# Kernel tuning notes

Measured on AMD Instinct MI355X. Metric: run time of the kernel, lower is better.

Reference implementation:

```python
import jax, jax.numpy as jnp
import numpy as np

HEADS, DIM_HEAD, NEIGHBORS = 8, 64, 64
REL_DIST_SCALE, REL_DIST_CUTOFF, THETA, EPS = 100.0, 5000.0, 10000.0, 1e-8


def _rotate_half(x):
    # interleaved pairs: (x0,x1),(x2,x3),... -> (-x1,x0),(-x3,x2),...
    xp = x.reshape(*x.shape[:-1], -1, 2)
    a, b = xp[..., 0], xp[..., 1]
    return jnp.stack((-b, a), axis=-1).reshape(x.shape)


def _apply_rotary(t, freqs):
    return t * jnp.cos(freqs) + _rotate_half(t) * jnp.sin(freqs)


def _gelu(x):
    return jax.nn.gelu(x, approximate=False)  # torch nn.GELU default = exact erf


def setup_inputs() -> dict:
    key = jax.random.key(0)
    ks = jax.random.split(key, 12)
    b, n, d, e = 2, 2048, 256, 16
    h, dh = HEADS, DIM_HEAD
    inner = h * dh
    std = 0.02
    return {
        "feats": jax.random.normal(ks[0], (b, n, d), jnp.float32),
        "coors": jax.random.normal(ks[1], (b, n, 3), jnp.float32),
        "edges": jax.random.normal(ks[2], (b, n, n, e), jnp.float32),
        "W_qkv": jax.random.normal(ks[3], (d, inner * 3), jnp.float32) * std,
        "W_out": jax.random.normal(ks[4], (inner, d), jnp.float32) * std,
        "b_out": jnp.zeros((d,), jnp.float32),
        "W_e1": jax.random.normal(ks[5], (h + e, 2 * (h + e)), jnp.float32) * std,
        "b_e1": jnp.zeros((2 * (h + e),), jnp.float32),
        "W_e2": jax.random.normal(ks[6], (2 * (h + e), h), jnp.float32) * std,
        "b_e2": jnp.zeros((h,), jnp.float32),
        "W_c": jax.random.normal(ks[7], (h, h), jnp.float32) * std,
        "b_c": jnp.zeros((h,), jnp.float32),
        "W_g": jax.random.normal(ks[8], (h, h), jnp.float32) * std,
        "b_g": jnp.zeros((h,), jnp.float32),
        "coors_combine": jax.random.normal(ks[9], (h,), jnp.float32),
        "coors_scale": jnp.ones((1,), jnp.float32),
    }


def reference(feats, coors, edges, W_qkv, W_out, b_out, W_e1, b_e1, W_e2, b_e2,
              W_c, b_c, W_g, b_g, coors_combine, coors_scale):
    b, n, d = feats.shape
    h, dh, nn_k = HEADS, DIM_HEAD, NEIGHBORS

    # pairwise relative coordinates / distances (O(n^2) irregular part)
    rel_coors = coors[:, :, None, :] - coors[:, None, :, :]            # b n n 3
    rel_dist = jnp.linalg.norm(rel_coors, axis=-1)                      # b n n

    # topk nearest neighbors (largest=False -> top_k of negated distances)
    _, nbhd_idx = jax.lax.top_k(-rel_dist, nn_k)                        # b n nn

    qkv = feats @ W_qkv                                                 # b n 3*h*dh
    q, k, v = jnp.split(qkv, 3, axis=-1)
    q = q.reshape(b, n, h, dh).transpose(0, 2, 1, 3)                    # b h n dh
    k = k.reshape(b, n, h, dh).transpose(0, 2, 1, 3)
    v = v.reshape(b, n, h, dh).transpose(0, 2, 1, 3)

    # batched_index_select gathers
    k = jax.vmap(lambda kb, ib: kb[:, ib])(k, nbhd_idx)                 # b h n nn dh
    v = jax.vmap(lambda vb, ib: vb[:, ib])(v, nbhd_idx)                 # b h n nn dh
    rel_dist_nb = jnp.take_along_axis(rel_dist, nbhd_idx, axis=2)       # b n nn
    rel_coors_nb = jnp.take_along_axis(rel_coors, nbhd_idx[..., None], axis=2)  # b n nn 3
    edges_nb = jnp.take_along_axis(edges, nbhd_idx[..., None], axis=2)  # b n nn e

    # rotary on relative distances; q's freqs are zeros -> identity rotation (skipped)
    inv_freq = 1.0 / (THETA ** (jnp.arange(0, dh, 2, dtype=jnp.float32) / dh))
    t = jnp.minimum(rel_dist_nb * REL_DIST_SCALE, REL_DIST_CUTOFF)
    freqs = jnp.repeat(t[..., None] * inv_freq, 2, axis=-1)[:, None]    # b 1 n nn dh
    k = _apply_rotary(k, freqs)
    v = _apply_rotary(v, freqs)

    # edges provided -> no 1/sqrt(dh) scale, then edge MLP
    qk = jnp.einsum('bhid,bhijd->bhij', q, k)                           # b h i j
    qk = jnp.transpose(qk, (0, 2, 3, 1))                                # b i j h
    x = jnp.concatenate([qk, edges_nb], axis=-1)                        # b i j (h+e)
    qk = _gelu(x @ W_e1 + b_e1) @ W_e2 + b_e2                           # b i j h

    # coordinate attention branch (coors_mlp = GELU + Linear when edges exist)
    coor_weights = _gelu(qk) @ W_c + b_c                                # b i j h
    coor_attn = jax.nn.softmax(coor_weights, axis=2)                    # softmax over j
    gate = jnp.tanh(qk @ W_g + b_g)                                     # b i j h

    nrm = jnp.linalg.norm(rel_coors_nb, axis=-1, keepdims=True)
    rel_normed = rel_coors_nb / jnp.maximum(nrm, EPS) * coors_scale     # b i j 3

    rel_out = jnp.einsum('bijh,bijc->bich', coor_attn * gate, rel_normed)
    coors_delta = jnp.einsum('bich,h->bic', rel_out, coors_combine)     # b n 3

    # feature attention branch
    attn = jax.nn.softmax(jnp.transpose(qk, (0, 3, 1, 2)), axis=-1)     # b h i j
    out = jnp.einsum('bhij,bhijd->bhid', attn, v)
    out = out.transpose(0, 2, 1, 3).reshape(b, n, h * dh)
    node_out = out @ W_out + b_out                                      # b n d
    return node_out, coors_delta
```

## Files before the change

kernel.cpp:

```cpp
#include <hip/hip_runtime.h>
#include <hip/hip_fp16.h>
#include <math.h>

#define NPTS 2048
#define NB 64
#define H 8
#define DH 64
#define INNER 512

__device__ __forceinline__ float gelu_exact(float x) {
  return 0.5f * x * (1.0f + erff(x * 0.7071067811865475f));
}

__device__ __forceinline__ unsigned int pack_cs(float c, float s) {
  __half2 h = __floats2half2_rn(c, s);
  return *reinterpret_cast<unsigned int*>(&h);
}
__device__ __forceinline__ float2 unpack_cs(unsigned int u) {
  __half2 h = *reinterpret_cast<__half2*>(&u);
  return __half22float2(h);
}

__global__ __launch_bounds__(256) void topk_kernel(const float* __restrict__ coors,
                                                   int* __restrict__ nbhd) {
  const int row = blockIdx.x;
  const int b = row >> 11;
  const int tid = threadIdx.x;
  __shared__ unsigned long long red[4];
  __shared__ unsigned long long winner;
  const float* cb = coors + (size_t)b * NPTS * 3;
  const float cx = coors[(size_t)row * 3 + 0];
  const float cy = coors[(size_t)row * 3 + 1];
  const float cz = coors[(size_t)row * 3 + 2];
  unsigned long long keys[8];
#pragma unroll
  for (int s = 0; s < 8; ++s) {
    const int j = tid + (s << 8);
    const float dx = cx - cb[j * 3 + 0];
    const float dy = cy - cb[j * 3 + 1];
    const float dz = cz - cb[j * 3 + 2];
    const float d = sqrtf(dx * dx + dy * dy + dz * dz);
    keys[s] = (((unsigned long long)__float_as_uint(d)) << 32) | (unsigned long long)j;
  }
  for (int it = 0; it < NB; ++it) {
    unsigned long long k = ~0ull;
#pragma unroll
    for (int s = 0; s < 8; ++s) k = keys[s] < k ? keys[s] : k;
#pragma unroll
    for (int off = 32; off > 0; off >>= 1) {
      unsigned long long o = __shfl_xor(k, off, 64);
      k = o < k ? o : k;
    }
    if ((tid & 63) == 0) red[tid >> 6] = k;
    __syncthreads();
    if (tid == 0) {
      unsigned long long w = red[0];
      for (int q = 1; q < 4; ++q) w = red[q] < w ? red[q] : w;
      winner = w;
      nbhd[(size_t)row * NB + it] = (int)(w & 0xffffffffull);
    }
    __syncthreads();
    const unsigned long long w = winner;
#pragma unroll
    for (int s = 0; s < 8; ++s)
      if (keys[s] == w) keys[s] = ~0ull;
  }
}

__global__ __launch_bounds__(256) void gemm_tiled(const float* __restrict__ A,
                                                  const float* __restrict__ B,
                                                  const float* __restrict__ bias,
                                                  float* __restrict__ C,
                                                  int M, int N, int K) {
  __shared__ float As[16][68];
  __shared__ float Bs[16][68];
  const int tid = threadIdx.x;
  const int tx = tid & 15;
  const int ty = tid >> 4;
  const int n0 = blockIdx.x << 6;
  const int m0 = blockIdx.y << 6;
  const int la_m = tid >> 2;
  const int la_k = (tid & 3) << 2;
  const int lb_k = tid >> 4;
  const int lb_n = (tid & 15) << 2;
  float acc[4][4] = {{0.f}};
  for (int kk = 0; kk < K; kk += 16) {
    const float4 a4 = *(const float4*)(A + (size_t)(m0 + la_m) * K + kk + la_k);
    const float4 b4 = *(const float4*)(B + (size_t)(kk + lb_k) * N + n0 + lb_n);
    As[la_k + 0][la_m] = a4.x;
    As[la_k + 1][la_m] = a4.y;
    As[la_k + 2][la_m] = a4.z;
    As[la_k + 3][la_m] = a4.w;
    *(float4*)(&Bs[lb_k][lb_n]) = b4;
    __syncthreads();
#pragma unroll
    for (int k = 0; k < 16; ++k) {
      const float4 av = *(const float4*)(&As[k][ty << 2]);
      const float4 bv = *(const float4*)(&Bs[k][tx << 2]);
      acc[0][0] += av.x * bv.x; acc[0][1] += av.x * bv.y; acc[0][2] += av.x * bv.z; acc[0][3] += av.x * bv.w;
      acc[1][0] += av.y * bv.x; acc[1][1] += av.y * bv.y; acc[1][2] += av.y * bv.z; acc[1][3] += av.y * bv.w;
      acc[2][0] += av.z * bv.x; acc[2][1] += av.z * bv.y; acc[2][2] += av.z * bv.z; acc[2][3] += av.z * bv.w;
      acc[3][0] += av.w * bv.x; acc[3][1] += av.w * bv.y; acc[3][2] += av.w * bv.z; acc[3][3] += av.w * bv.w;
    }
    __syncthreads();
  }
#pragma unroll
  for (int r = 0; r < 4; ++r) {
#pragma unroll
    for (int c = 0; c < 4; ++c) {
      const int n = n0 + (tx << 2) + c;
      float v = acc[r][c];
      if (bias) v += bias[n];
      C[(size_t)(m0 + (ty << 2) + r) * N + n] = v;
    }
  }
}

__global__ __launch_bounds__(256, 4) void attn_kernel(
    const float* __restrict__ qkv, const float* __restrict__ coors,
    const float* __restrict__ edges, const int* __restrict__ nbhd,
    const float* __restrict__ W_e1, const float* __restrict__ b_e1,
    const float* __restrict__ W_e2, const float* __restrict__ b_e2,
    const float* __restrict__ W_c, const float* __restrict__ b_c,
    const float* __restrict__ W_g, const float* __restrict__ b_g,
    const float* __restrict__ coors_combine, const float* __restrict__ coors_scale,
    float* __restrict__ attn_out, float* __restrict__ coors_out) {
  __shared__ float q_s[H][68];
  __shared__ unsigned int cs_s[NB][33];
  __shared__ float qk_s[NB][9];
  __shared__ float qk2_s[NB][9];
  __shared__ float attn_s[NB][9];
  __shared__ float edg_s[NB][17];
  __shared__ float rel_s[NB][4];
  __shared__ float dist_s[NB];
  __shared__ int idx_s[NB];
  __shared__ float We1[24 * 48];
  __shared__ float We2[48 * 9];
  __shared__ float be1[48];
  __shared__ float be2[H], bcs[H], bgs[H], ccs[H];
  __shared__ float Wcs[H * H], Wgs[H * H];
  __shared__ float invf[32];
  __shared__ float credx[4][3];

  const int row = blockIdx.x;
  const int b = row >> 11;
  const int tid = threadIdx.x;
  const size_t qbase = (size_t)row * 1536;

  {
    int t0 = tid;
    q_s[t0 >> 6][t0 & 63] = qkv[qbase + t0];
    int t1 = tid + 256;
    q_s[t1 >> 6][t1 & 63] = qkv[qbase + t1];
  }
  for (int t = tid; t < 24 * 48; t += 256) We1[t] = W_e1[t];
  for (int t = tid; t < 48 * H; t += 256) We2[(t >> 3) * 9 + (t & 7)] = W_e2[t];
  if (tid < 48) be1[tid] = b_e1[tid];
  if (tid < H) { be2[tid] = b_e2[tid]; bcs[tid] = b_c[tid]; bgs[tid] = b_g[tid]; ccs[tid] = coors_combine[tid]; }
  if (tid < H * H) { Wcs[tid] = W_c[tid]; Wgs[tid] = W_g[tid]; }
  if (tid < 32) invf[tid] = expf(-(float)tid * 0.28782313662425575f);
  if (tid < NB) {
    const int jj = nbhd[(size_t)row * NB + tid];
    idx_s[tid] = jj;
    const float csc = coors_scale[0];
    const float dx = coors[(size_t)row * 3 + 0] - coors[((size_t)b * NPTS + jj) * 3 + 0];
    const float dy = coors[(size_t)row * 3 + 1] - coors[((size_t)b * NPTS + jj) * 3 + 1];
    const float dz = coors[(size_t)row * 3 + 2] - coors[((size_t)b * NPTS + jj) * 3 + 2];
    const float d = sqrtf(dx * dx + dy * dy + dz * dz);
    dist_s[tid] = d;
    const float inv = csc / fmaxf(d, 1e-8f);
    rel_s[tid][0] = dx * inv;
    rel_s[tid][1] = dy * inv;
    rel_s[tid][2] = dz * inv;
  }
  __syncthreads();

#pragma unroll
  for (int s = 0; s < 8; ++s) {
    const int p = tid + (s << 8);
    const int j = p >> 5, m = p & 31;
    const float t = fminf(dist_s[j] * 100.0f, 5000.0f);
    float sv, cv;
    __sincosf(t * invf[m], &sv, &cv);
    cs_s[j][m] = pack_cs(cv, sv);
  }
  {
    const size_t ebase = (size_t)row * NPTS * 16;
#pragma unroll
    for (int s = 0; s < 4; ++s) {
      const int p = tid + (s << 8);
      const int j = p >> 4, e = p & 15;
      edg_s[j][e] = edges[ebase + (size_t)idx_s[j] * 16 + e];
    }
  }
  __syncthreads();

#pragma unroll
  for (int s = 0; s < 2; ++s) {
    const int p = tid + (s << 8);
    const int j = p >> 3, h = p & 7;
    const float* krow = qkv + ((size_t)b * NPTS + idx_s[j]) * 1536 + INNER + h * DH;
    float acc = 0.f;
#pragma unroll
    for (int m4 = 0; m4 < 16; ++m4) {
      const float4 kv = *(const float4*)(krow + (m4 << 2));
      const float4 qv = *(const float4*)(&q_s[h][m4 << 2]);
      const int m = m4 << 1;
      const float2 c0 = unpack_cs(cs_s[j][m]);
      const float2 c1 = unpack_cs(cs_s[j][m + 1]);
      acc += qv.x * (kv.x * c0.x - kv.y * c0.y) + qv.y * (kv.y * c0.x + kv.x * c0.y) +
             qv.z * (kv.z * c1.x - kv.w * c1.y) + qv.w * (kv.w * c1.x + kv.z * c1.y);
    }
    qk_s[j][h] = acc;
  }
  __syncthreads();

  {
    const int j = tid >> 2, part = tid & 3;
    float hv[12];
#pragma unroll
    for (int l = 0; l < 12; ++l) {
      const int hh = part * 12 + l;
      float a = be1[hh];
#pragma unroll
      for (int r = 0; r < 8; ++r) a += qk_s[j][r] * We1[r * 48 + hh];
#pragma unroll
      for (int r = 0; r < 16; ++r) a += edg_s[j][r] * We1[(8 + r) * 48 + hh];
      hv[l] = gelu_exact(a);
    }
    float p8[8];
#pragma unroll
    for (int h = 0; h < 8; ++h) {
      float a = 0.f;
#pragma unroll
      for (int l = 0; l < 12; ++l) a += hv[l] * We2[(part * 12 + l) * 9 + h];
      a += __shfl_xor(a, 1, 64);
      a += __shfl_xor(a, 2, 64);
      p8[h] = a + be2[h];
    }
    qk2_s[j][(part << 1) + 0] = p8[(part << 1) + 0];
    qk2_s[j][(part << 1) + 1] = p8[(part << 1) + 1];
  }
  __syncthreads();

  {
    const int lane = tid & 63;
    const int wv = tid >> 6;
    float qv[8], ge[8];
#pragma unroll
    for (int r = 0; r < 8; ++r) { qv[r] = qk2_s[lane][r]; ge[r] = gelu_exact(qv[r]); }
    float wpart = 0.f;
#pragma unroll
    for (int hh = 0; hh < 2; ++hh) {
      const int h = (wv << 1) + hh;
      float y = qv[h];
      float my = y;
#pragma unroll
      for (int off = 32; off > 0; off >>= 1) my = fmaxf(my, __shfl_xor(my, off, 64));
      const float e2 = __expf(y - my);
      float s2 = e2;
#pragma unroll
      for (int off = 32; off > 0; off >>= 1) s2 += __shfl_xor(s2, off, 64);
      attn_s[lane][h] = e2 / s2;
      float cwv = bcs[h], gt = bgs[h];
#pragma unroll
      for (int r = 0; r < 8; ++r) {
        cwv += ge[r] * Wcs[r * 8 + h];
        gt += qv[r] * Wgs[r * 8 + h];
      }
      gt = tanhf(gt);
      float mx = cwv;
#pragma unroll
      for (int off = 32; off > 0; off >>= 1) mx = fmaxf(mx, __shfl_xor(mx, off, 64));
      const float e = __expf(cwv - mx);
      float sm = e;
#pragma unroll
      for (int off = 32; off > 0; off >>= 1) sm += __shfl_xor(sm, off, 64);
      wpart += (e / sm) * gt * ccs[h];
    }
    float px = wpart * rel_s[lane][0];
    float py = wpart * rel_s[lane][1];
    float pz = wpart * rel_s[lane][2];
#pragma unroll
    for (int off = 32; off > 0; off >>= 1) {
      px += __shfl_xor(px, off, 64);
      py += __shfl_xor(py, off, 64);
      pz += __shfl_xor(pz, off, 64);
    }
    if (lane == 0) { credx[wv][0] = px; credx[wv][1] = py; credx[wv][2] = pz; }
  }
  __syncthreads();

  if (tid == 0) {
    coors_out[(size_t)row * 3 + 0] = credx[0][0] + credx[1][0] + credx[2][0] + credx[3][0];
    coors_out[(size_t)row * 3 + 1] = credx[0][1] + credx[1][1] + credx[2][1] + credx[3][1];
    coors_out[(size_t)row * 3 + 2] = credx[0][2] + credx[1][2] + credx[2][2] + credx[3][2];
  }

  {
    const int h = tid >> 5, m = tid & 31;
    const size_t off_v = (size_t)(2 * INNER + h * DH + (m << 1));
    float o0 = 0.f, o1 = 0.f;
#pragma unroll 8
    for (int j = 0; j < NB; ++j) {
      const float2 v = *(const float2*)(qkv + ((size_t)b * NPTS + idx_s[j]) * 1536 + off_v);
      const float2 cs = unpack_cs(cs_s[j][m]);
      const float a = attn_s[j][h];
      o0 += a * (v.x * cs.x - v.y * cs.y);
      o1 += a * (v.y * cs.x + v.x * cs.y);
    }
    *(float2*)(attn_out + (size_t)row * INNER + h * DH + (m << 1)) = make_float2(o0, o1);
  }
}

extern "C" void kernel_launch(void* const* d_in, const int* in_sizes, int n_in,
                              void* d_out, int out_size, void* d_ws, size_t ws_size,
                              hipStream_t stream) {
  const float* feats = (const float*)d_in[0];
  const float* coors = (const float*)d_in[1];
  const float* edges = (const float*)d_in[2];
  const float* W_qkv = (const float*)d_in[3];
  const float* W_out = (const float*)d_in[4];
  const float* b_out = (const float*)d_in[5];
  const float* W_e1 = (const float*)d_in[6];
  const float* b_e1 = (const float*)d_in[7];
  const float* W_e2 = (const float*)d_in[8];
  const float* b_e2 = (const float*)d_in[9];
  const float* W_c = (const float*)d_in[10];
  const float* b_c = (const float*)d_in[11];
  const float* W_g = (const float*)d_in[12];
  const float* b_g = (const float*)d_in[13];
  const float* cc = (const float*)d_in[14];
  const float* cscale = (const float*)d_in[15];

  float* out = (float*)d_out;
  float* qkv = (float*)d_ws;
  float* attn_out = qkv + (size_t)4096 * 1536;
  int* nbhd = (int*)(attn_out + (size_t)4096 * 512);

  gemm_tiled<<<dim3(24, 64), 256, 0, stream>>>(feats, W_qkv, nullptr, qkv, 4096, 1536, 256);
  topk_kernel<<<4096, 256, 0, stream>>>(coors, nbhd);
  attn_kernel<<<4096, 256, 0, stream>>>(qkv, coors, edges, nbhd,
                                        W_e1, b_e1, W_e2, b_e2, W_c, b_c, W_g, b_g,
                                        cc, cscale, attn_out, out + (size_t)4096 * 256);
  gemm_tiled<<<dim3(4, 64), 256, 0, stream>>>(attn_out, W_out, b_out, out, 4096, 256, 512);
}
```

Measured before the change: 1.004 ms.

## Restructure top-k as per-wave sorted selection plus merge-by-rank

Each thread sorts its 8 distance keys with a sorting network. Each wave then independently extracts its 64 smallest keys by repeated shuffle-min and pop, with no block-wide barriers per iteration. A single sync follows, and the four per-wave sorted lists are merged by computing each candidate's global rank with binary searches into the other lists. This removes 128 __syncthreads and the serial single-thread reduction from the top-k loop, in exchange for more register shuffling and a merge step.

```diff
diff --git a/kernel.cpp b/kernel.cpp
--- a/kernel.cpp
+++ b/kernel.cpp
@@ -26,44 +26,68 @@
   const int row = blockIdx.x;
   const int b = row >> 11;
   const int tid = threadIdx.x;
-  __shared__ unsigned long long red[4];
-  __shared__ unsigned long long winner;
+  const int lane = tid & 63;
+  const int wv = tid >> 6;
+  __shared__ unsigned long long list[4][64];
+
   const float* cb = coors + (size_t)b * NPTS * 3;
   const float cx = coors[(size_t)row * 3 + 0];
   const float cy = coors[(size_t)row * 3 + 1];
   const float cz = coors[(size_t)row * 3 + 2];
+
   unsigned long long keys[8];
 #pragma unroll
   for (int s = 0; s < 8; ++s) {
-    const int j = tid + (s << 8);
+    const int j = (wv << 9) + (s << 6) + lane;
     const float dx = cx - cb[j * 3 + 0];
     const float dy = cy - cb[j * 3 + 1];
     const float dz = cz - cb[j * 3 + 2];
     const float d = sqrtf(dx * dx + dy * dy + dz * dz);
     keys[s] = (((unsigned long long)__float_as_uint(d)) << 32) | (unsigned long long)j;
   }
-  for (int it = 0; it < NB; ++it) {
-    unsigned long long k = ~0ull;
-#pragma unroll
-    for (int s = 0; s < 8; ++s) k = keys[s] < k ? keys[s] : k;
+
+#define CAS(a, b)                                                   \
+  {                                                                 \
+    unsigned long long lo = keys[a] < keys[b] ? keys[a] : keys[b];  \
+    unsigned long long hi = keys[a] < keys[b] ? keys[b] : keys[a];  \
+    keys[a] = lo; keys[b] = hi;                                     \
+  }
+  CAS(0, 1) CAS(2, 3) CAS(4, 5) CAS(6, 7)
+  CAS(0, 2) CAS(1, 3) CAS(4, 6) CAS(5, 7)
+  CAS(1, 2) CAS(5, 6)
+  CAS(0, 4) CAS(1, 5) CAS(2, 6) CAS(3, 7)
+  CAS(2, 4) CAS(3, 5)
+  CAS(1, 2) CAS(3, 4) CAS(5, 6)
+#undef CAS
+
+  for (int r = 0; r < NB; ++r) {
+    unsigned long long w = keys[0];
 #pragma unroll
     for (int off = 32; off > 0; off >>= 1) {
-      unsigned long long o = __shfl_xor(k, off, 64);
-      k = o < k ? o : k;
-    }
-    if ((tid & 63) == 0) red[tid >> 6] = k;
-    __syncthreads();
-    if (tid == 0) {
-      unsigned long long w = red[0];
-      for (int q = 1; q < 4; ++q) w = red[q] < w ? red[q] : w;
-      winner = w;
-      nbhd[(size_t)row * NB + it] = (int)(w & 0xffffffffull);
-    }
-    __syncthreads();
-    const unsigned long long w = winner;
-#pragma unroll
-    for (int s = 0; s < 8; ++s)
-      if (keys[s] == w) keys[s] = ~0ull;
+      unsigned long long o = __shfl_xor(w, off, 64);
+      w = o < w ? o : w;
+    }
+    const bool win = (keys[0] == w);
+#pragma unroll
+    for (int i = 0; i < 7; ++i) keys[i] = win ? keys[i + 1] : keys[i];
+    keys[7] = win ? ~0ull : keys[7];
+    if (lane == (r & 63)) list[wv][r] = w;
+  }
+  __syncthreads();
+
+  {
+    const unsigned long long c = list[wv][lane];
+    int rank = lane;
+#pragma unroll
+    for (int o = 1; o < 4; ++o) {
+      const unsigned long long* L = list[(wv + o) & 3];
+      int base = 0;
+#pragma unroll
+      for (int sz = 32; sz > 0; sz >>= 1)
+        if (L[base + sz - 1] < c) base += sz;
+      rank += base;
+    }
+    if (rank < NB) nbhd[(size_t)row * NB + rank] = (int)(c & 0xffffffffull);
   }
 }
 
```

Measured after the change: 1.002 ms. About the same (-0.2%).
